# Optimization experiments

Hardware: AMD Instinct MI355X
Metric: run time of the kernel (lower is better)

The kernel has to match this reference:

```python
import jax, jax.numpy as jnp
import numpy as np
from jax import lax

DEPTH, STACKS = 8, 2
C, SK, OUT = 64, 256, 256          # res_channels, skip_channels, out_channels
NB = DEPTH * STACKS                 # 16 blocks
DILS = [2 ** i for i in range(DEPTH)] * STACKS


def causal_conv(x, w, dil):
    # x: [B,C,T], w: [2C,C,2]; causal: left-pad by dil, kernel size 2 dilated
    return lax.conv_general_dilated(
        x, w, window_strides=(1,), padding=[(dil, 0)], rhs_dilation=(dil,),
        dimension_numbers=('NCH', 'OIH', 'NCH'))


def conv1x1(x, w):
    # x: [B,c_in,T], w: [c_out,c_in]
    return jnp.einsum('oc,bct->bot', w, x)


def setup_inputs() -> dict:
    key = jax.random.key(0)
    ks = jax.random.split(key, 8)
    B, T = 4, 8192
    x = jax.random.randint(ks[0], (B, T), 0, 256)
    h = jax.random.normal(ks[1], (B, NB * 2 * C, T), dtype=jnp.float32)
    embed = jax.random.normal(ks[2], (256, C), dtype=jnp.float32) * 0.1
    w_conv = jax.random.normal(ks[3], (NB, 2 * C, C, 2), dtype=jnp.float32) * 0.08
    w_res = jax.random.normal(ks[4], (NB, C, C), dtype=jnp.float32) * 0.08
    w_skip = jax.random.normal(ks[5], (NB, SK, C), dtype=jnp.float32) * 0.08
    w_out1 = jax.random.normal(ks[6], (OUT, SK), dtype=jnp.float32) * 0.05
    w_out2 = jax.random.normal(ks[7], (OUT, OUT), dtype=jnp.float32) * 0.05
    return {'x': x, 'h': h, 'embed': embed, 'w_conv': w_conv,
            'w_res': w_res, 'w_skip': w_skip, 'w_out1': w_out1, 'w_out2': w_out2}


def reference(x, h, embed, w_conv, w_res, w_skip, w_out1, w_out2):
    out = embed[x].transpose(0, 2, 1)          # [B,C,T]
    hs = jnp.split(h, NB, axis=1)              # NB chunks of [B,2C,T]
    skip = None
    for i in range(NB):
        g = causal_conv(out, w_conv[i], DILS[i]) + hs[i]   # [B,2C,T]
        z = jnp.tanh(g[:, :C]) * jax.nn.sigmoid(g[:, C:])  # gated activation
        s = conv1x1(z, w_skip[i])                          # [B,SK,T]
        skip = s if skip is None else skip + s
        if i < NB - 1:  # last block has return_residual=False (skip only)
            out = out + conv1x1(z, w_res[i])
    y = jax.nn.relu(skip)
    y = jax.nn.relu(conv1x1(y, w_out1))
    return conv1x1(y, w_out2)                  # [B,OUT,T]
```

## Files before the change

kernel.cpp:

```cpp
#include <hip/hip_runtime.h>

#define NB 16
#define TT 8192
#define Bb 4

typedef __attribute__((ext_vector_type(8))) short short8;
typedef __attribute__((ext_vector_type(16))) float f32x16;

__device__ __forceinline__ unsigned short bf16_rn(float f) {
  unsigned int u = __float_as_uint(f);
  u += 0x7FFF + ((u >> 16) & 1);
  return (unsigned short)(u >> 16);
}
__device__ __forceinline__ unsigned int pack2(float a, float b) {
  return (unsigned int)bf16_rn(a) | ((unsigned int)bf16_rn(b) << 16);
}
__device__ __forceinline__ int kpos(int k) {
  int g = (k >> 2) & 1;
  int e = (k & 3) + 4 * (k >> 3);
  return g * 8 + e;
}
__device__ __forceinline__ int kinv(int p) {
  int g = p >> 3, e = p & 7;
  return (e & 3) + 4 * g + 8 * (e >> 2);
}

__global__ __launch_bounds__(256) void prep_weights(
    const float* __restrict__ wconv, const float* __restrict__ wres,
    const float* __restrict__ wsk, const float* __restrict__ w1,
    const float* __restrict__ w2, short* __restrict__ dwc,
    short* __restrict__ dwr, short* __restrict__ dws,
    short* __restrict__ dw1, short* __restrict__ dw2)
{
  int i = blockIdx.x * 256 + threadIdx.x;
  if (i < 262144) {
    int k = kinv(i & 15);
    int ic = (i & 48) | k;
    int oc = (i >> 6) & 127;
    int tap = (i >> 13) & 1;
    int blk = i >> 14;
    dwc[i] = (short)bf16_rn(wconv[(((blk * 128 + oc) * 64 + ic) << 1) | tap]);
    return;
  }
  int j = i - 262144;
  if (j < 65536) { dwr[j] = (short)bf16_rn(wres[(j & ~15) | kinv(j & 15)]); return; }
  j -= 65536;
  if (j < 262144) { dws[j] = (short)bf16_rn(wsk[(j & ~15) | kinv(j & 15)]); return; }
  j -= 262144;
  if (j < 65536) { dw1[j] = (short)bf16_rn(w1[(j & ~15) | kinv(j & 15)]); return; }
  j -= 65536;
  if (j < 65536) { dw2[j] = (short)bf16_rn(w2[(j & ~15) | kinv(j & 15)]); return; }
}

__global__ __launch_bounds__(128) void block_kernel(
    const float* __restrict__ rin, float* __restrict__ rout,
    const int* __restrict__ x, const float* __restrict__ embed,
    const float* __restrict__ h, const short* __restrict__ wc,
    const short* __restrict__ wr, unsigned short* __restrict__ zg,
    int blk, int dil, int last)
{
  __shared__ short win[160 * 64];
  __shared__ float rs[32 * 64];
  __shared__ short zl[32 * 64];

  const int b = blockIdx.y;
  const int t0 = blockIdx.x * 32;
  const int tid = threadIdx.x;
  const int lane = tid & 63, wv = tid >> 6;
  const int l31 = lane & 31, hi = lane >> 5;

  const int tcol = t0 + l31;
  f32x16 aA, aS;
  const float* hb = h + ((size_t)b * 2048 + (size_t)blk * 128) * TT;
#pragma unroll
  for (int r = 0; r < 16; ++r) {
    int row = (r & 3) + 4 * hi + 8 * (r >> 2) + 32 * wv;
    aA[r] = hb[(size_t)row * TT + tcol];
    aS[r] = hb[(size_t)(row + 64) * TT + tcol];
  }

  if (blk == 0) {
    const int* xb = x + b * TT;
#pragma unroll
    for (int it = 0; it < 8; ++it) {
      int u = it * 128 + tid;
      int cpair = u & 31, t = u >> 5;
      int c0 = cpair * 2;
      int xi = xb[t0 + t];
      float v0 = embed[(size_t)xi * 64 + c0];
      float v1 = embed[(size_t)xi * 64 + c0 + 1];
      rs[t * 64 + c0] = v0;
      rs[t * 64 + c0 + 1] = v1;
      int p0 = (c0 & 48) | kpos(c0 & 15);
      int w = dil + t;
      unsigned int byte = (unsigned int)(w * 128 + p0 * 2) ^
                          (unsigned int)((w & 7) << 4);
      *(unsigned int*)((char*)win + byte) = pack2(v0, v1);
    }
    if (tid < 32) {
      int c0 = tid * 2;
      float v0 = 0.f, v1 = 0.f;
      if (t0 > 0) {
        int xi = xb[t0 - 1];
        v0 = embed[(size_t)xi * 64 + c0];
        v1 = embed[(size_t)xi * 64 + c0 + 1];
      }
      int p0 = (c0 & 48) | kpos(c0 & 15);
      unsigned int byte = (unsigned int)(p0 * 2);
      *(unsigned int*)((char*)win + byte) = pack2(v0, v1);
    }
  } else {
    const float* rbase = rin + (size_t)b * TT * 64;
#pragma unroll
    for (int it = 0; it < 8; ++it) {
      int u = it * 128 + tid;
      int cpair = u & 31, t = u >> 5;
      int c0 = cpair * 2;
      float2 f = *(const float2*)(rbase + (size_t)(t0 + t) * 64 + c0);
      rs[t * 64 + c0] = f.x;
      rs[t * 64 + c0 + 1] = f.y;
      int p0 = (c0 & 48) | kpos(c0 & 15);
      int w = dil + t;
      unsigned int byte = (unsigned int)(w * 128 + p0 * 2) ^
                          (unsigned int)((w & 7) << 4);
      *(unsigned int*)((char*)win + byte) = pack2(f.x, f.y);
    }
    for (int u = tid; u < dil * 32; u += 128) {
      int cpair = u & 31, w = u >> 5;
      int c0 = cpair * 2;
      int gt = t0 - dil + w;
      float2 f = {0.f, 0.f};
      if (gt >= 0) f = *(const float2*)(rbase + (size_t)gt * 64 + c0);
      int p0 = (c0 & 48) | kpos(c0 & 15);
      unsigned int byte = (unsigned int)(w * 128 + p0 * 2) ^
                          (unsigned int)((w & 7) << 4);
      *(unsigned int*)((char*)win + byte) = pack2(f.x, f.y);
    }
  }
  __syncthreads();

  const short* wA0 = wc + (size_t)blk * 16384 + (32 * wv + l31) * 64;
  const short* wA1 = wA0 + 8192;
  const int r1 = dil + l31;
  const int r0 = l31;
#pragma unroll
  for (int ks = 0; ks < 4; ++ks) {
    int off = ks * 16 + 8 * hi;
    short8 b1 = *(const short8*)((char*)win +
        ((unsigned int)(r1 * 128 + off * 2) ^ (unsigned int)((r1 & 7) << 4)));
    short8 b0 = *(const short8*)((char*)win +
        ((unsigned int)(r0 * 128 + off * 2) ^ (unsigned int)((r0 & 7) << 4)));
    short8 a0t = *(const short8*)(wA0 + off);
    short8 a1t = *(const short8*)(wA1 + off);
    short8 a0s = *(const short8*)(wA0 + 4096 + off);
    short8 a1s = *(const short8*)(wA1 + 4096 + off);
    aA = __builtin_amdgcn_mfma_f32_32x32x16_bf16(a0t, b0, aA, 0, 0, 0);
    aA = __builtin_amdgcn_mfma_f32_32x32x16_bf16(a1t, b1, aA, 0, 0, 0);
    aS = __builtin_amdgcn_mfma_f32_32x32x16_bf16(a0s, b0, aS, 0, 0, 0);
    aS = __builtin_amdgcn_mfma_f32_32x32x16_bf16(a1s, b1, aS, 0, 0, 0);
  }

#pragma unroll
  for (int r = 0; r < 16; r += 2) {
    int ic0 = (r & 3) + 4 * hi + 8 * (r >> 2) + 32 * wv;
    float z0 = (1.f - 2.f / (__expf(2.f * aA[r]) + 1.f)) *
               (1.f / (1.f + __expf(-aS[r])));
    float z1 = (1.f - 2.f / (__expf(2.f * aA[r + 1]) + 1.f)) *
               (1.f / (1.f + __expf(-aS[r + 1])));
    int p = (ic0 & ~15) | kpos(ic0 & 15);
    int tloc = l31;
    unsigned int byte = (unsigned int)(tloc * 128 + p * 2) ^
                        (unsigned int)((tloc & 7) << 4);
    *(unsigned int*)((char*)zl + byte) = pack2(z0, z1);
  }
  __syncthreads();

  {
    unsigned short* zb = zg + ((size_t)(blk * Bb + b) * TT + t0) * 64;
#pragma unroll
    for (int it = 0; it < 8; ++it) {
      int u = it * 128 + tid;
      int p2 = u & 31, t = u >> 5;
      unsigned int byte = (unsigned int)(t * 128 + p2 * 4) ^
                          (unsigned int)((t & 7) << 4);
      unsigned int v = *(const unsigned int*)((char*)zl + byte);
      *(unsigned int*)(zb + (size_t)t * 64 + p2 * 2) = v;
    }
  }

  if (!last) {
    const int trow = l31;
    f32x16 ar = {};
    const short* wrb = wr + (size_t)blk * 4096 + (wv * 32 + l31) * 64;
#pragma unroll
    for (int ks = 0; ks < 4; ++ks) {
      int off = ks * 16 + 8 * hi;
      short8 az = *(const short8*)((char*)zl +
          ((unsigned int)(trow * 128 + off * 2) ^ (unsigned int)((trow & 7) << 4)));
      short8 bw = *(const short8*)(wrb + off);
      ar = __builtin_amdgcn_mfma_f32_32x32x16_bf16(az, bw, ar, 0, 0, 0);
    }
    float* obase = rout + (size_t)b * TT * 64;
    int oc = wv * 32 + l31;
#pragma unroll
    for (int r = 0; r < 16; ++r) {
      int t = (r & 3) + 4 * hi + 8 * (r >> 2);
      obase[(size_t)(t0 + t) * 64 + oc] = rs[t * 64 + oc] + ar[r];
    }
  }
}

__global__ __launch_bounds__(256) void head_kernel(
    const unsigned short* __restrict__ zg, const short* __restrict__ wsk,
    const short* __restrict__ w1, const short* __restrict__ w2,
    float* __restrict__ out)
{
  __shared__ short zbuf[2][32 * 64];
  __shared__ short yb[32 * 256];
  __shared__ short y2b[32 * 256];

  const int b = blockIdx.y;
  const int t0 = blockIdx.x * 32;
  const int tid = threadIdx.x;
  const int lane = tid & 63, wv = tid >> 6;
  const int l31 = lane & 31, hi = lane >> 5;

  {
#pragma unroll
    for (int it = 0; it < 4; ++it) {
      int u = it * 256 + tid;
      int p2 = u & 31, t = u >> 5;
      unsigned int v = *(const unsigned int*)(zg +
          ((size_t)(0 * Bb + b) * TT + t0 + t) * 64 + p2 * 2);
      unsigned int byte = (unsigned int)(t * 128 + p2 * 4) ^
                          (unsigned int)((t & 7) << 4);
      *(unsigned int*)((char*)zbuf[0] + byte) = v;
    }
  }

  f32x16 acc0 = {}, acc1 = {};
  const short* wsb0 = wsk + (wv * 32 + l31) * 64;
  const short* wsb1 = wsk + ((wv + 4) * 32 + l31) * 64;

  for (int blk = 0; blk < NB; ++blk) {
    __syncthreads();
    if (blk < NB - 1) {
#pragma unroll
      for (int it = 0; it < 4; ++it) {
        int u = it * 256 + tid;
        int p2 = u & 31, t = u >> 5;
        unsigned int v = *(const unsigned int*)(zg +
            ((size_t)((blk + 1) * Bb + b) * TT + t0 + t) * 64 + p2 * 2);
        unsigned int byte = (unsigned int)(t * 128 + p2 * 4) ^
                            (unsigned int)((t & 7) << 4);
        *(unsigned int*)((char*)zbuf[(blk + 1) & 1] + byte) = v;
      }
    }
    const short* zb = zbuf[blk & 1];
#pragma unroll
    for (int ks = 0; ks < 4; ++ks) {
      int off = ks * 16 + 8 * hi;
      short8 bw0 = *(const short8*)(wsb0 + (size_t)blk * 16384 + off);
      short8 bw1 = *(const short8*)(wsb1 + (size_t)blk * 16384 + off);
      short8 az = *(const short8*)((char*)zb +
          ((unsigned int)(l31 * 128 + off * 2) ^ (unsigned int)((l31 & 7) << 4)));
      acc0 = __builtin_amdgcn_mfma_f32_32x32x16_bf16(az, bw0, acc0, 0, 0, 0);
      acc1 = __builtin_amdgcn_mfma_f32_32x32x16_bf16(az, bw1, acc1, 0, 0, 0);
    }
  }

  {
    int sk0 = wv * 32 + l31;
    int sk1 = sk0 + 128;
    int p0 = (sk0 & 0xF0) | kpos(sk0 & 15);
    int p1 = (sk1 & 0xF0) | kpos(sk1 & 15);
#pragma unroll
    for (int r = 0; r < 16; ++r) {
      int dt = (r & 3) + 4 * hi + 8 * (r >> 2);
      unsigned int b0 = (unsigned int)(dt * 512 + p0 * 2) ^
                        (unsigned int)((dt & 7) << 4);
      unsigned int b1 = (unsigned int)(dt * 512 + p1 * 2) ^
                        (unsigned int)((dt & 7) << 4);
      *(short*)((char*)yb + b0) = (short)bf16_rn(fmaxf(acc0[r], 0.f));
      *(short*)((char*)yb + b1) = (short)bf16_rn(fmaxf(acc1[r], 0.f));
    }
  }
  __syncthreads();

#pragma unroll
  for (int ot = 0; ot < 2; ++ot) {
    const short* w1r = w1 + ((wv + 4 * ot) * 32 + l31) * 256;
    const int trow = l31;
    f32x16 acc = {};
#pragma unroll
    for (int ks = 0; ks < 16; ++ks) {
      int off = ks * 16 + 8 * hi;
      short8 by = *(const short8*)((char*)yb +
          ((unsigned int)(trow * 512 + off * 2) ^ (unsigned int)((trow & 7) << 4)));
      short8 aw = *(const short8*)(w1r + off);
      acc = __builtin_amdgcn_mfma_f32_32x32x16_bf16(aw, by, acc, 0, 0, 0);
    }
#pragma unroll
    for (int r = 0; r < 16; r += 2) {
      int o0 = (wv + 4 * ot) * 32 + (r & 3) + 4 * hi + 8 * (r >> 2);
      unsigned int v = (unsigned int)bf16_rn(fmaxf(acc[r], 0.f)) |
                       ((unsigned int)bf16_rn(fmaxf(acc[r + 1], 0.f)) << 16);
      int p = (o0 & 0xF0) | kpos(o0 & 15);
      unsigned int byte = (unsigned int)(trow * 512 + p * 2) ^
                          (unsigned int)((trow & 7) << 4);
      *(unsigned int*)((char*)y2b + byte) = v;
    }
  }
  __syncthreads();

  {
    float* ob = out + (size_t)b * 256 * TT;
#pragma unroll
    for (int ot = 0; ot < 2; ++ot) {
      const short* w2r = w2 + ((wv + 4 * ot) * 32 + l31) * 256;
      const int trow = l31;
      f32x16 acc = {};
#pragma unroll
      for (int ks = 0; ks < 16; ++ks) {
        int off = ks * 16 + 8 * hi;
        short8 by = *(const short8*)((char*)y2b +
            ((unsigned int)(trow * 512 + off * 2) ^ (unsigned int)((trow & 7) << 4)));
        short8 aw = *(const short8*)(w2r + off);
        acc = __builtin_amdgcn_mfma_f32_32x32x16_bf16(aw, by, acc, 0, 0, 0);
      }
#pragma unroll
      for (int r = 0; r < 16; ++r) {
        int oc = (wv + 4 * ot) * 32 + (r & 3) + 4 * hi + 8 * (r >> 2);
        ob[(size_t)oc * TT + t0 + trow] = acc[r];
      }
    }
  }
}

extern "C" void kernel_launch(void* const* d_in, const int* in_sizes, int n_in,
                              void* d_out, int out_size, void* d_ws, size_t ws_size,
                              hipStream_t stream)
{
  const int* x = (const int*)d_in[0];
  const float* h = (const float*)d_in[1];
  const float* embed = (const float*)d_in[2];
  const float* w_conv = (const float*)d_in[3];
  const float* w_res = (const float*)d_in[4];
  const float* w_skip = (const float*)d_in[5];
  const float* w_out1 = (const float*)d_in[6];
  const float* w_out2 = (const float*)d_in[7];
  float* out = (float*)d_out;

  char* ws = (char*)d_ws;
  float* resid0 = (float*)ws;
  float* resid1 = (float*)(ws + (size_t)(8 << 20));
  unsigned short* zg = (unsigned short*)(ws + (size_t)(16 << 20));
  short* dwc = (short*)(ws + (size_t)(80 << 20));
  short* dwr = dwc + 262144;
  short* dws = dwr + 65536;
  short* dw1 = dws + 262144;
  short* dw2 = dw1 + 65536;

  prep_weights<<<2816, 256, 0, stream>>>(w_conv, w_res, w_skip, w_out1, w_out2,
                                         dwc, dwr, dws, dw1, dw2);

  float* rf[2] = {resid0, resid1};
  const int dils[NB] = {1, 2, 4, 8, 16, 32, 64, 128,
                        1, 2, 4, 8, 16, 32, 64, 128};
  for (int i = 0; i < NB; ++i) {
    block_kernel<<<dim3(TT / 32, Bb), 128, 0, stream>>>(
        rf[i & 1], rf[(i + 1) & 1], x, embed, h, dwc, dwr, zg,
        i, dils[i], i == NB - 1);
  }

  head_kernel<<<dim3(TT / 32, Bb), 256, 0, stream>>>(zg, dws, dw1, dw2, out);
}
```

Measured before the change: 384.0 us.

## Fuse pairs of small-dilation residual blocks into one kernel with halo recompute

Adds a pair_kernel that runs two consecutive WaveNet blocks in one launch. It recomputes the first block over the halo rows the second block's dilated conv needs, so the intermediate residual stays in shared memory. This replaces six pairs of launches and their residual round-trips through global memory for dilations up to 32. The cost is redundant MFMA and gate work for the halo columns, extra h loads, and larger shared memory per workgroup, which may lower occupancy.

```diff
diff --git a/kernel.cpp b/kernel.cpp
--- a/kernel.cpp
+++ b/kernel.cpp
@@ -24,6 +24,11 @@
   int g = p >> 3, e = p & 7;
   return (e & 3) + 4 * g + 8 * (e >> 2);
 }
+
+#define WINRD(base, r, off)                                                    \
+  (*(const short8*)((char*)(base) +                                            \
+      (((unsigned int)((r) * 128 + (off) * 2)) ^                               \
+       ((unsigned int)(((r) & 7) << 4)))))
 
 __global__ __launch_bounds__(256) void prep_weights(
     const float* __restrict__ wconv, const float* __restrict__ wres,
@@ -54,7 +59,6 @@
 
 __global__ __launch_bounds__(128) void block_kernel(
     const float* __restrict__ rin, float* __restrict__ rout,
-    const int* __restrict__ x, const float* __restrict__ embed,
     const float* __restrict__ h, const short* __restrict__ wc,
     const short* __restrict__ wr, unsigned short* __restrict__ zg,
     int blk, int dil, int last)
@@ -79,63 +83,31 @@
     aS[r] = hb[(size_t)(row + 64) * TT + tcol];
   }
 
-  if (blk == 0) {
-    const int* xb = x + b * TT;
-#pragma unroll
-    for (int it = 0; it < 8; ++it) {
-      int u = it * 128 + tid;
-      int cpair = u & 31, t = u >> 5;
-      int c0 = cpair * 2;
-      int xi = xb[t0 + t];
-      float v0 = embed[(size_t)xi * 64 + c0];
-      float v1 = embed[(size_t)xi * 64 + c0 + 1];
-      rs[t * 64 + c0] = v0;
-      rs[t * 64 + c0 + 1] = v1;
-      int p0 = (c0 & 48) | kpos(c0 & 15);
-      int w = dil + t;
-      unsigned int byte = (unsigned int)(w * 128 + p0 * 2) ^
-                          (unsigned int)((w & 7) << 4);
-      *(unsigned int*)((char*)win + byte) = pack2(v0, v1);
-    }
-    if (tid < 32) {
-      int c0 = tid * 2;
-      float v0 = 0.f, v1 = 0.f;
-      if (t0 > 0) {
-        int xi = xb[t0 - 1];
-        v0 = embed[(size_t)xi * 64 + c0];
-        v1 = embed[(size_t)xi * 64 + c0 + 1];
-      }
-      int p0 = (c0 & 48) | kpos(c0 & 15);
-      unsigned int byte = (unsigned int)(p0 * 2);
-      *(unsigned int*)((char*)win + byte) = pack2(v0, v1);
-    }
-  } else {
-    const float* rbase = rin + (size_t)b * TT * 64;
-#pragma unroll
-    for (int it = 0; it < 8; ++it) {
-      int u = it * 128 + tid;
-      int cpair = u & 31, t = u >> 5;
-      int c0 = cpair * 2;
-      float2 f = *(const float2*)(rbase + (size_t)(t0 + t) * 64 + c0);
-      rs[t * 64 + c0] = f.x;
-      rs[t * 64 + c0 + 1] = f.y;
-      int p0 = (c0 & 48) | kpos(c0 & 15);
-      int w = dil + t;
-      unsigned int byte = (unsigned int)(w * 128 + p0 * 2) ^
-                          (unsigned int)((w & 7) << 4);
-      *(unsigned int*)((char*)win + byte) = pack2(f.x, f.y);
-    }
-    for (int u = tid; u < dil * 32; u += 128) {
-      int cpair = u & 31, w = u >> 5;
-      int c0 = cpair * 2;
-      int gt = t0 - dil + w;
-      float2 f = {0.f, 0.f};
-      if (gt >= 0) f = *(const float2*)(rbase + (size_t)gt * 64 + c0);
-      int p0 = (c0 & 48) | kpos(c0 & 15);
-      unsigned int byte = (unsigned int)(w * 128 + p0 * 2) ^
-                          (unsigned int)((w & 7) << 4);
-      *(unsigned int*)((char*)win + byte) = pack2(f.x, f.y);
-    }
+  const float* rbase = rin + (size_t)b * TT * 64;
+#pragma unroll
+  for (int it = 0; it < 8; ++it) {
+    int u = it * 128 + tid;
+    int cpair = u & 31, t = u >> 5;
+    int c0 = cpair * 2;
+    float2 f = *(const float2*)(rbase + (size_t)(t0 + t) * 64 + c0);
+    rs[t * 64 + c0] = f.x;
+    rs[t * 64 + c0 + 1] = f.y;
+    int p0 = (c0 & 48) | kpos(c0 & 15);
+    int w = dil + t;
+    unsigned int byte = (unsigned int)(w * 128 + p0 * 2) ^
+                        (unsigned int)((w & 7) << 4);
+    *(unsigned int*)((char*)win + byte) = pack2(f.x, f.y);
+  }
+  for (int u = tid; u < dil * 32; u += 128) {
+    int cpair = u & 31, w = u >> 5;
+    int c0 = cpair * 2;
+    int gt = t0 - dil + w;
+    float2 f = {0.f, 0.f};
+    if (gt >= 0) f = *(const float2*)(rbase + (size_t)gt * 64 + c0);
+    int p0 = (c0 & 48) | kpos(c0 & 15);
+    unsigned int byte = (unsigned int)(w * 128 + p0 * 2) ^
+                        (unsigned int)((w & 7) << 4);
+    *(unsigned int*)((char*)win + byte) = pack2(f.x, f.y);
   }
   __syncthreads();
 
@@ -146,10 +118,8 @@
 #pragma unroll
   for (int ks = 0; ks < 4; ++ks) {
     int off = ks * 16 + 8 * hi;
-    short8 b1 = *(const short8*)((char*)win +
-        ((unsigned int)(r1 * 128 + off * 2) ^ (unsigned int)((r1 & 7) << 4)));
-    short8 b0 = *(const short8*)((char*)win +
-        ((unsigned int)(r0 * 128 + off * 2) ^ (unsigned int)((r0 & 7) << 4)));
+    short8 b1 = WINRD(win, r1, off);
+    short8 b0 = WINRD(win, r0, off);
     short8 a0t = *(const short8*)(wA0 + off);
     short8 a1t = *(const short8*)(wA1 + off);
     short8 a0s = *(const short8*)(wA0 + 4096 + off);
@@ -195,8 +165,7 @@
 #pragma unroll
     for (int ks = 0; ks < 4; ++ks) {
       int off = ks * 16 + 8 * hi;
-      short8 az = *(const short8*)((char*)zl +
-          ((unsigned int)(trow * 128 + off * 2) ^ (unsigned int)((trow & 7) << 4)));
+      short8 az = WINRD(zl, trow, off);
       short8 bw = *(const short8*)(wrb + off);
       ar = __builtin_amdgcn_mfma_f32_32x32x16_bf16(az, bw, ar, 0, 0, 0);
     }
@@ -206,6 +175,263 @@
     for (int r = 0; r < 16; ++r) {
       int t = (r & 3) + 4 * hi + 8 * (r >> 2);
       obase[(size_t)(t0 + t) * 64 + oc] = rs[t * 64 + oc] + ar[r];
+    }
+  }
+}
+
+__global__ __launch_bounds__(128) void pair_kernel(
+    const float* __restrict__ rin, float* __restrict__ rout,
+    const int* __restrict__ x, const float* __restrict__ embed,
+    const float* __restrict__ h, const short* __restrict__ wc,
+    const short* __restrict__ wr, unsigned short* __restrict__ zg,
+    int blk0, int d0, int d1, int first)
+{
+  __shared__ short win0[80 * 64];
+  __shared__ float rsx[64 * 64];
+  __shared__ short win1[64 * 64];
+  __shared__ short zlA[32 * 64];
+  __shared__ short zlB[32 * 64];
+  __shared__ short zl1[32 * 64];
+
+  const int b = blockIdx.y;
+  const int t0 = blockIdx.x * 32;
+  const int tid = threadIdx.x;
+  const int lane = tid & 63, wv = tid >> 6;
+  const int l31 = lane & 31, hi = lane >> 5;
+
+  const int N0 = 32 + d0 + d1;
+  const int N1 = 32 + d1;
+  const int g0 = t0 - d0 - d1;
+  const int g1 = t0 - d1;
+
+  f32x16 aAB, aSB, aAA, aSA;
+  const float* hb0 = h + ((size_t)b * 2048 + (size_t)blk0 * 128) * TT;
+  const int cB = t0 + l31;
+  const int cA = t0 - d1 + l31;
+  const bool useA = (l31 < d1) && (cA >= 0);
+#pragma unroll
+  for (int r = 0; r < 16; ++r) {
+    int row = (r & 3) + 4 * hi + 8 * (r >> 2) + 32 * wv;
+    aAB[r] = hb0[(size_t)row * TT + cB];
+    aSB[r] = hb0[(size_t)(row + 64) * TT + cB];
+    aAA[r] = useA ? hb0[(size_t)row * TT + cA] : 0.f;
+    aSA[r] = useA ? hb0[(size_t)(row + 64) * TT + cA] : 0.f;
+  }
+
+  if (first) {
+    const int* xb = x + b * TT;
+    for (int u = tid; u < N0 * 32; u += 128) {
+      int cpair = u & 31, w = u >> 5, c0 = cpair * 2;
+      int gt = g0 + w;
+      float v0 = 0.f, v1 = 0.f;
+      if (gt >= 0) {
+        int xi = xb[gt];
+        v0 = embed[(size_t)xi * 64 + c0];
+        v1 = embed[(size_t)xi * 64 + c0 + 1];
+      }
+      int p0 = (c0 & 48) | kpos(c0 & 15);
+      unsigned int byte = (unsigned int)(w * 128 + p0 * 2) ^
+                          (unsigned int)((w & 7) << 4);
+      *(unsigned int*)((char*)win0 + byte) = pack2(v0, v1);
+    }
+    for (int u = tid; u < N1 * 32; u += 128) {
+      int cpair = u & 31, w = u >> 5, c0 = cpair * 2;
+      int gt = g1 + w;
+      float v0 = 0.f, v1 = 0.f;
+      if (gt >= 0) {
+        int xi = xb[gt];
+        v0 = embed[(size_t)xi * 64 + c0];
+        v1 = embed[(size_t)xi * 64 + c0 + 1];
+      }
+      rsx[w * 64 + c0] = v0;
+      rsx[w * 64 + c0 + 1] = v1;
+    }
+  } else {
+    const float* rbase = rin + (size_t)b * TT * 64;
+    for (int u = tid; u < N0 * 32; u += 128) {
+      int cpair = u & 31, w = u >> 5, c0 = cpair * 2;
+      int gt = g0 + w;
+      float2 f = {0.f, 0.f};
+      if (gt >= 0) f = *(const float2*)(rbase + (size_t)gt * 64 + c0);
+      int p0 = (c0 & 48) | kpos(c0 & 15);
+      unsigned int byte = (unsigned int)(w * 128 + p0 * 2) ^
+                          (unsigned int)((w & 7) << 4);
+      *(unsigned int*)((char*)win0 + byte) = pack2(f.x, f.y);
+    }
+    for (int u = tid; u < N1 * 32; u += 128) {
+      int cpair = u & 31, w = u >> 5, c0 = cpair * 2;
+      int gt = g1 + w;
+      float2 f = {0.f, 0.f};
+      if (gt >= 0) f = *(const float2*)(rbase + (size_t)gt * 64 + c0);
+      rsx[w * 64 + c0] = f.x;
+      rsx[w * 64 + c0 + 1] = f.y;
+    }
+  }
+  __syncthreads();
+
+  {
+    const short* wA0 = wc + (size_t)blk0 * 16384 + (32 * wv + l31) * 64;
+    const short* wA1 = wA0 + 8192;
+    const int rA1 = d0 + l31, rA0 = l31;
+    const int rB1 = d0 + d1 + l31, rB0 = d1 + l31;
+#pragma unroll
+    for (int ks = 0; ks < 4; ++ks) {
+      int off = ks * 16 + 8 * hi;
+      short8 a0t = *(const short8*)(wA0 + off);
+      short8 a1t = *(const short8*)(wA1 + off);
+      short8 a0s = *(const short8*)(wA0 + 4096 + off);
+      short8 a1s = *(const short8*)(wA1 + 4096 + off);
+      short8 bA1 = WINRD(win0, rA1, off);
+      short8 bA0 = WINRD(win0, rA0, off);
+      short8 bB1 = WINRD(win0, rB1, off);
+      short8 bB0 = WINRD(win0, rB0, off);
+      aAA = __builtin_amdgcn_mfma_f32_32x32x16_bf16(a0t, bA0, aAA, 0, 0, 0);
+      aAA = __builtin_amdgcn_mfma_f32_32x32x16_bf16(a1t, bA1, aAA, 0, 0, 0);
+      aSA = __builtin_amdgcn_mfma_f32_32x32x16_bf16(a0s, bA0, aSA, 0, 0, 0);
+      aSA = __builtin_amdgcn_mfma_f32_32x32x16_bf16(a1s, bA1, aSA, 0, 0, 0);
+      aAB = __builtin_amdgcn_mfma_f32_32x32x16_bf16(a0t, bB0, aAB, 0, 0, 0);
+      aAB = __builtin_amdgcn_mfma_f32_32x32x16_bf16(a1t, bB1, aAB, 0, 0, 0);
+      aSB = __builtin_amdgcn_mfma_f32_32x32x16_bf16(a0s, bB0, aSB, 0, 0, 0);
+      aSB = __builtin_amdgcn_mfma_f32_32x32x16_bf16(a1s, bB1, aSB, 0, 0, 0);
+    }
+  }
+
+#pragma unroll
+  for (int r = 0; r < 16; r += 2) {
+    int ic0 = (r & 3) + 4 * hi + 8 * (r >> 2) + 32 * wv;
+    int p = (ic0 & ~15) | kpos(ic0 & 15);
+    unsigned int byte = (unsigned int)(l31 * 128 + p * 2) ^
+                        (unsigned int)((l31 & 7) << 4);
+    float zA0 = (1.f - 2.f / (__expf(2.f * aAA[r]) + 1.f)) *
+                (1.f / (1.f + __expf(-aSA[r])));
+    float zA1 = (1.f - 2.f / (__expf(2.f * aAA[r + 1]) + 1.f)) *
+                (1.f / (1.f + __expf(-aSA[r + 1])));
+    *(unsigned int*)((char*)zlA + byte) = pack2(zA0, zA1);
+    float zB0 = (1.f - 2.f / (__expf(2.f * aAB[r]) + 1.f)) *
+                (1.f / (1.f + __expf(-aSB[r])));
+    float zB1 = (1.f - 2.f / (__expf(2.f * aAB[r + 1]) + 1.f)) *
+                (1.f / (1.f + __expf(-aSB[r + 1])));
+    *(unsigned int*)((char*)zlB + byte) = pack2(zB0, zB1);
+  }
+  __syncthreads();
+
+  {
+    unsigned short* zb = zg + ((size_t)(blk0 * Bb + b) * TT + t0) * 64;
+#pragma unroll
+    for (int it = 0; it < 8; ++it) {
+      int u = it * 128 + tid;
+      int p2 = u & 31, t = u >> 5;
+      unsigned int byte = (unsigned int)(t * 128 + p2 * 4) ^
+                          (unsigned int)((t & 7) << 4);
+      unsigned int v = *(const unsigned int*)((char*)zlB + byte);
+      *(unsigned int*)(zb + (size_t)t * 64 + p2 * 2) = v;
+    }
+  }
+
+  {
+    const short* wrb = wr + (size_t)blk0 * 4096 + (wv * 32 + l31) * 64;
+    f32x16 arA = {}, arB = {};
+#pragma unroll
+    for (int ks = 0; ks < 4; ++ks) {
+      int off = ks * 16 + 8 * hi;
+      short8 bw = *(const short8*)(wrb + off);
+      short8 azA = WINRD(zlA, l31, off);
+      short8 azB = WINRD(zlB, l31, off);
+      arA = __builtin_amdgcn_mfma_f32_32x32x16_bf16(azA, bw, arA, 0, 0, 0);
+      arB = __builtin_amdgcn_mfma_f32_32x32x16_bf16(azB, bw, arB, 0, 0, 0);
+    }
+    int oc = wv * 32 + l31;
+    int ocp = (oc & 48) | kpos(oc & 15);
+#pragma unroll
+    for (int r = 0; r < 16; ++r) {
+      int lt = (r & 3) + 4 * hi + 8 * (r >> 2);
+      float oB = rsx[(d1 + lt) * 64 + oc] + arB[r];
+      rsx[(d1 + lt) * 64 + oc] = oB;
+      unsigned int byteB = (unsigned int)((d1 + lt) * 128 + ocp * 2) ^
+                           (unsigned int)(((d1 + lt) & 7) << 4);
+      *(short*)((char*)win1 + byteB) = (short)bf16_rn(oB);
+      if (lt < d1) {
+        float oA = rsx[lt * 64 + oc] + arA[r];
+        unsigned int byteA = (unsigned int)(lt * 128 + ocp * 2) ^
+                             (unsigned int)((lt & 7) << 4);
+        *(short*)((char*)win1 + byteA) = (short)bf16_rn(oA);
+      }
+    }
+  }
+
+  f32x16 aA1, aS1;
+  const float* hb1 = hb0 + (size_t)128 * TT;
+#pragma unroll
+  for (int r = 0; r < 16; ++r) {
+    int row = (r & 3) + 4 * hi + 8 * (r >> 2) + 32 * wv;
+    aA1[r] = hb1[(size_t)row * TT + cB];
+    aS1[r] = hb1[(size_t)(row + 64) * TT + cB];
+  }
+  __syncthreads();
+
+  {
+    const short* wB0 = wc + (size_t)(blk0 + 1) * 16384 + (32 * wv + l31) * 64;
+    const short* wB1 = wB0 + 8192;
+    const int r1 = d1 + l31, r0 = l31;
+#pragma unroll
+    for (int ks = 0; ks < 4; ++ks) {
+      int off = ks * 16 + 8 * hi;
+      short8 b1 = WINRD(win1, r1, off);
+      short8 b0 = WINRD(win1, r0, off);
+      short8 a0t = *(const short8*)(wB0 + off);
+      short8 a1t = *(const short8*)(wB1 + off);
+      short8 a0s = *(const short8*)(wB0 + 4096 + off);
+      short8 a1s = *(const short8*)(wB1 + 4096 + off);
+      aA1 = __builtin_amdgcn_mfma_f32_32x32x16_bf16(a0t, b0, aA1, 0, 0, 0);
+      aA1 = __builtin_amdgcn_mfma_f32_32x32x16_bf16(a1t, b1, aA1, 0, 0, 0);
+      aS1 = __builtin_amdgcn_mfma_f32_32x32x16_bf16(a0s, b0, aS1, 0, 0, 0);
+      aS1 = __builtin_amdgcn_mfma_f32_32x32x16_bf16(a1s, b1, aS1, 0, 0, 0);
+    }
+  }
+
+#pragma unroll
+  for (int r = 0; r < 16; r += 2) {
+    int ic0 = (r & 3) + 4 * hi + 8 * (r >> 2) + 32 * wv;
+    float z0 = (1.f - 2.f / (__expf(2.f * aA1[r]) + 1.f)) *
+               (1.f / (1.f + __expf(-aS1[r])));
+    float z1 = (1.f - 2.f / (__expf(2.f * aA1[r + 1]) + 1.f)) *
+               (1.f / (1.f + __expf(-aS1[r + 1])));
+    int p = (ic0 & ~15) | kpos(ic0 & 15);
+    unsigned int byte = (unsigned int)(l31 * 128 + p * 2) ^
+                        (unsigned int)((l31 & 7) << 4);
+    *(unsigned int*)((char*)zl1 + byte) = pack2(z0, z1);
+  }
+  __syncthreads();
+
+  {
+    unsigned short* zb = zg + ((size_t)((blk0 + 1) * Bb + b) * TT + t0) * 64;
+#pragma unroll
+    for (int it = 0; it < 8; ++it) {
+      int u = it * 128 + tid;
+      int p2 = u & 31, t = u >> 5;
+      unsigned int byte = (unsigned int)(t * 128 + p2 * 4) ^
+                          (unsigned int)((t & 7) << 4);
+      unsigned int v = *(const unsigned int*)((char*)zl1 + byte);
+      *(unsigned int*)(zb + (size_t)t * 64 + p2 * 2) = v;
+    }
+  }
+
+  {
+    const short* wrb = wr + (size_t)(blk0 + 1) * 4096 + (wv * 32 + l31) * 64;
+    f32x16 ar = {};
+#pragma unroll
+    for (int ks = 0; ks < 4; ++ks) {
+      int off = ks * 16 + 8 * hi;
+      short8 az = WINRD(zl1, l31, off);
+      short8 bw = *(const short8*)(wrb + off);
+      ar = __builtin_amdgcn_mfma_f32_32x32x16_bf16(az, bw, ar, 0, 0, 0);
+    }
+    float* obase = rout + (size_t)b * TT * 64;
+    int oc = wv * 32 + l31;
+#pragma unroll
+    for (int r = 0; r < 16; ++r) {
+      int lt = (r & 3) + 4 * hi + 8 * (r >> 2);
+      obase[(size_t)(t0 + lt) * 64 + oc] = rsx[(d1 + lt) * 64 + oc] + ar[r];
     }
   }
 }
@@ -262,8 +488,7 @@
       int off = ks * 16 + 8 * hi;
       short8 bw0 = *(const short8*)(wsb0 + (size_t)blk * 16384 + off);
       short8 bw1 = *(const short8*)(wsb1 + (size_t)blk * 16384 + off);
-      short8 az = *(const short8*)((char*)zb +
-          ((unsigned int)(l31 * 128 + off * 2) ^ (unsigned int)((l31 & 7) << 4)));
+      short8 az = WINRD(zb, l31, off);
       acc0 = __builtin_amdgcn_mfma_f32_32x32x16_bf16(az, bw0, acc0, 0, 0, 0);
       acc1 = __builtin_amdgcn_mfma_f32_32x32x16_bf16(az, bw1, acc1, 0, 0, 0);
     }
@@ -352,8 +577,8 @@
   float* out = (float*)d_out;
 
   char* ws = (char*)d_ws;
-  float* resid0 = (float*)ws;
-  float* resid1 = (float*)(ws + (size_t)(8 << 20));
+  float* r0 = (float*)ws;
+  float* r1 = (float*)(ws + (size_t)(8 << 20));
   unsigned short* zg = (unsigned short*)(ws + (size_t)(16 << 20));
   short* dwc = (short*)(ws + (size_t)(80 << 20));
   short* dwr = dwc + 262144;
@@ -364,14 +589,24 @@
   prep_weights<<<2816, 256, 0, stream>>>(w_conv, w_res, w_skip, w_out1, w_out2,
                                          dwc, dwr, dws, dw1, dw2);
 
-  float* rf[2] = {resid0, resid1};
-  const int dils[NB] = {1, 2, 4, 8, 16, 32, 64, 128,
-                        1, 2, 4, 8, 16, 32, 64, 128};
-  for (int i = 0; i < NB; ++i) {
-    block_kernel<<<dim3(TT / 32, Bb), 128, 0, stream>>>(
-        rf[i & 1], rf[(i + 1) & 1], x, embed, h, dwc, dwr, zg,
-        i, dils[i], i == NB - 1);
-  }
-
-  head_kernel<<<dim3(TT / 32, Bb), 256, 0, stream>>>(zg, dws, dw1, dw2, out);
-}
+  const dim3 grid(TT / 32, Bb);
+
+  pair_kernel<<<grid, 128, 0, stream>>>(nullptr, r0, x, embed, h, dwc, dwr, zg,
+                                        0, 1, 2, 1);
+  pair_kernel<<<grid, 128, 0, stream>>>(r0, r1, x, embed, h, dwc, dwr, zg,
+                                        2, 4, 8, 0);
+  pair_kernel<<<grid, 128, 0, stream>>>(r1, r0, x, embed, h, dwc, dwr, zg,
+                                        4, 16, 32, 0);
+  block_kernel<<<grid, 128, 0, stream>>>(r0, r1, h, dwc, dwr, zg, 6, 64, 0);
+  block_kernel<<<grid, 128, 0, stream>>>(r1, r0, h, dwc, dwr, zg, 7, 128, 0);
+  pair_kernel<<<grid, 128, 0, stream>>>(r0, r1, x, embed, h, dwc, dwr, zg,
+                                        8, 1, 2, 0);
+  pair_kernel<<<grid, 128, 0, stream>>>(r1, r0, x, embed, h, dwc, dwr, zg,
+                                        10, 4, 8, 0);
+  pair_kernel<<<grid, 128, 0, stream>>>(r0, r1, x, embed, h, dwc, dwr, zg,
+                                        12, 16, 32, 0);
+  block_kernel<<<grid, 128, 0, stream>>>(r1, r0, h, dwc, dwr, zg, 14, 64, 0);
+  block_kernel<<<grid, 128, 0, stream>>>(r0, r1, h, dwc, dwr, zg, 15, 128, 1);
+
+  head_kernel<<<grid, 256, 0, stream>>>(zg, dws, dw1, dw2, out);
+}
```

Measured after the change: 458.0 us. 19.3% more time.
